# Performance work log

Measured on AMD Instinct MI355X. Metric: run time of the kernel, lower is better.

Reference implementation:

```python
import jax, jax.numpy as jnp
import numpy as np

N_NODES = 100000
N_EDGES = 640000
IN_CH = 128
OUT_CH = 128


def setup_inputs() -> dict:
    key = jax.random.key(0)
    k1, k2, k3, k4, k5, k6 = jax.random.split(key, 6)
    row = jax.random.randint(k1, (N_EDGES,), 0, N_NODES, dtype=jnp.int64 if jax.config.jax_enable_x64 else jnp.int32)
    col = jax.random.randint(k2, (N_EDGES,), 0, N_NODES, dtype=jnp.int64 if jax.config.jax_enable_x64 else jnp.int32)
    vals = jax.random.uniform(k3, (N_EDGES,), dtype=jnp.float32)
    X = jax.random.normal(k4, (N_NODES, IN_CH), dtype=jnp.float32)
    weights = jax.random.normal(k5, (IN_CH, OUT_CH), dtype=jnp.float32)
    bias = jax.random.normal(k6, (OUT_CH,), dtype=jnp.float32)
    return {"row": row, "col": col, "vals": vals, "X": X, "weights": weights, "bias": bias}


def reference(row, col, vals, X, weights, bias):
    # A is sparse COO: A[row[e], col[e]] = vals[e]
    N = X.shape[0]
    # dense feature transform: [N, out]
    XTheta = X @ weights
    # D = (row_sum(A) + 1)^(-1/2)
    deg = jax.ops.segment_sum(vals, row, num_segments=N)
    D = jax.lax.rsqrt(deg + 1.0)
    # Xprime = D * (A @ (D * XTheta))
    Y = D[:, None] * XTheta                                    # [N, out]
    msgs = vals[:, None] * Y[col]                              # [E, out] gather
    AY = jax.ops.segment_sum(msgs, row, num_segments=N)        # [N, out] scatter-add
    return D[:, None] * AY + bias
```

## Files before the change

### kernel.cpp

```cpp
#include <hip/hip_runtime.h>
#include <hip/hip_bf16.h>


#define N_CH 128
#define WT_LD 136
#define FIXS 16777216.0f

typedef __attribute__((ext_vector_type(8))) short short8;
typedef __attribute__((ext_vector_type(4))) float f32x4;
typedef __attribute__((ext_vector_type(4))) unsigned short ushort4v;

__device__ inline unsigned short f2bf(float f) {
    unsigned u = __float_as_uint(f);
    return (unsigned short)((u + 0x7FFFu + ((u >> 16) & 1u)) >> 16);
}
__device__ inline float bf2f(unsigned short h) {
    return __uint_as_float(((unsigned)h) << 16);
}

__global__ __launch_bounds__(256) void rank_kernel(const int* __restrict__ row,
                                                   const float* __restrict__ vals,
                                                   unsigned long long* __restrict__ packed,
                                                   int* __restrict__ rank,
                                                   const float* __restrict__ W,
                                                   unsigned short* __restrict__ Wt,
                                                   int E, int rankBlocks) {
    if ((int)blockIdx.x >= rankBlocks) {
        int i = (blockIdx.x - rankBlocks) * 256 + threadIdx.x;
        int k = i >> 7, n = i & 127;
        Wt[n * N_CH + k] = f2bf(W[k * N_CH + n]);
        return;
    }
    int e0 = blockIdx.x * 512 + threadIdx.x;
#pragma unroll
    for (int j = 0; j < 2; ++j) {
        int e = e0 + j * 256;
        if (e < E) {
            int r = row[e];
            unsigned fx = (unsigned)(vals[e] * FIXS);
            unsigned long long old =
                atomicAdd(&packed[r], (1ULL << 32) | (unsigned long long)fx);
            rank[e] = (int)(old >> 32);
        }
    }
}

__global__ __launch_bounds__(256) void scan1_kernel(const unsigned long long* __restrict__ packed,
                                                    int* __restrict__ pos,
                                                    int* __restrict__ bsum, int N) {
    __shared__ int s[256];
    int t = threadIdx.x;
    int i = blockIdx.x * 256 + t;
    int v = (i < N) ? (int)(packed[i] >> 32) : 0;
    s[t] = v;
    __syncthreads();
    for (int off = 1; off < 256; off <<= 1) {
        int x = (t >= off) ? s[t - off] : 0;
        __syncthreads();
        s[t] += x;
        __syncthreads();
    }
    if (i < N) pos[i] = s[t] - v;
    if (t == 255) bsum[blockIdx.x] = s[t];
}

__global__ __launch_bounds__(256) void scan3_kernel(int* __restrict__ pos,
                                                    const int* __restrict__ bsum,
                                                    const unsigned long long* __restrict__ packed,
                                                    float* __restrict__ dinv, int N) {
    __shared__ int s[256];
    int t = threadIdx.x;
    int b = blockIdx.x;
    int acc = 0;
    for (int j = t; j < b; j += 256) acc += bsum[j];
    s[t] = acc;
    __syncthreads();
    for (int off = 128; off > 0; off >>= 1) {
        if (t < off) s[t] += s[t + off];
        __syncthreads();
    }
    int i = b * 256 + t;
    if (i < N) {
        pos[i] += s[0];
        float deg = (float)(unsigned)(packed[i] & 0xFFFFFFFFull) * (1.0f / FIXS);
        dinv[i] = rsqrtf(deg + 1.0f);
    }
}

__global__ __launch_bounds__(256) void gemm_place_kernel(
        const float* __restrict__ X, const unsigned short* __restrict__ Wt,
        const float* __restrict__ dinv, unsigned short* __restrict__ Ybf, int N,
        const int* __restrict__ row, const int* __restrict__ col,
        const float* __restrict__ vals, const int* __restrict__ pos,
        const int* __restrict__ rank, uint2* __restrict__ epack, int E,
        int gemmBlocks) {
    __shared__ unsigned short Wl[N_CH * WT_LD];

    if ((int)blockIdx.x >= gemmBlocks) {
        int e0 = (blockIdx.x - gemmBlocks) * 1024 + threadIdx.x;
#pragma unroll
        for (int j = 0; j < 4; ++j) {
            int e = e0 + j * 256;
            if (e < E) {
                int r = row[e];
                int p = pos[r] + rank[e];
                epack[p] = make_uint2((unsigned)col[e], __float_as_uint(vals[e]));
            }
        }
        return;
    }

    const int t = threadIdx.x;
    const short8* Wg = (const short8*)Wt;
#pragma unroll
    for (int j = 0; j < 8; ++j) {
        int idx = t + 256 * j;
        int r = idx >> 4, cc = idx & 15;
        *(short8*)(Wl + r * WT_LD + cc * 8) = Wg[idx];
    }
    __syncthreads();

    const int lane = t & 63;
    const int wv = t >> 6;
    const int m = lane & 15;
    const int q = lane >> 4;

#pragma unroll
    for (int i = 0; i < 2; ++i) {
        const int base = (blockIdx.x * 8 + wv * 2 + i) * 16;
        if (base >= N) break;

        short8 a[4];
        const float* xrow = X + (size_t)(base + m) * N_CH + q * 8;
#pragma unroll
        for (int c = 0; c < 4; ++c) {
            f32x4 lo = *(const f32x4*)(xrow + c * 32);
            f32x4 hi = *(const f32x4*)(xrow + c * 32 + 4);
            short8 v;
            v[0] = (short)f2bf(lo[0]); v[1] = (short)f2bf(lo[1]);
            v[2] = (short)f2bf(lo[2]); v[3] = (short)f2bf(lo[3]);
            v[4] = (short)f2bf(hi[0]); v[5] = (short)f2bf(hi[1]);
            v[6] = (short)f2bf(hi[2]); v[7] = (short)f2bf(hi[3]);
            a[c] = v;
        }

        f32x4 acc[8];
#pragma unroll
        for (int tt = 0; tt < 8; ++tt) acc[tt] = (f32x4){0.f, 0.f, 0.f, 0.f};

#pragma unroll
        for (int tt = 0; tt < 8; ++tt) {
            const unsigned short* wrow = Wl + (tt * 16 + m) * WT_LD + q * 8;
#pragma unroll
            for (int c = 0; c < 4; ++c) {
                short8 b = *(const short8*)(wrow + c * 32);
                acc[tt] = __builtin_amdgcn_mfma_f32_16x16x32_bf16(b, a[c], acc[tt], 0, 0, 0);
            }
        }

        const float d = dinv[base + m];
        unsigned short* yrow = Ybf + (size_t)(base + m) * N_CH;
#pragma unroll
        for (int tt = 0; tt < 8; ++tt) {
            unsigned lo = (unsigned)f2bf(acc[tt][0] * d) |
                          ((unsigned)f2bf(acc[tt][1] * d) << 16);
            unsigned hi = (unsigned)f2bf(acc[tt][2] * d) |
                          ((unsigned)f2bf(acc[tt][3] * d) << 16);
            *(uint2*)(yrow + tt * 16 + q * 4) = make_uint2(lo, hi);
        }
    }
}

__global__ __launch_bounds__(256) void gather_kernel(const int* __restrict__ pos,
                                                     const uint2* __restrict__ epack,
                                                     const unsigned short* __restrict__ Ybf,
                                                     const float* __restrict__ dinv,
                                                     const float* __restrict__ bias,
                                                     float* __restrict__ out, int N, int E) {
    unsigned gid = blockIdx.x * 256u + threadIdx.x;
    int n = gid >> 5;
    if (n >= N) return;
    int lane = gid & 31;
    int c = lane * 4;

    int e = pos[n];
    int end = (n + 1 < N) ? pos[n + 1] : E;

    float4 acc = make_float4(0.f, 0.f, 0.f, 0.f);
    for (; e + 4 <= end; e += 4) {
        uint2 p0 = epack[e + 0];
        uint2 p1 = epack[e + 1];
        uint2 p2 = epack[e + 2];
        uint2 p3 = epack[e + 3];
        ushort4v y0 = *(const ushort4v*)(Ybf + (size_t)p0.x * N_CH + c);
        ushort4v y1 = *(const ushort4v*)(Ybf + (size_t)p1.x * N_CH + c);
        ushort4v y2 = *(const ushort4v*)(Ybf + (size_t)p2.x * N_CH + c);
        ushort4v y3 = *(const ushort4v*)(Ybf + (size_t)p3.x * N_CH + c);
        float v0 = __uint_as_float(p0.y);
        float v1 = __uint_as_float(p1.y);
        float v2 = __uint_as_float(p2.y);
        float v3 = __uint_as_float(p3.y);
        acc.x += v0 * bf2f(y0[0]) + v1 * bf2f(y1[0]) + v2 * bf2f(y2[0]) + v3 * bf2f(y3[0]);
        acc.y += v0 * bf2f(y0[1]) + v1 * bf2f(y1[1]) + v2 * bf2f(y2[1]) + v3 * bf2f(y3[1]);
        acc.z += v0 * bf2f(y0[2]) + v1 * bf2f(y1[2]) + v2 * bf2f(y2[2]) + v3 * bf2f(y3[2]);
        acc.w += v0 * bf2f(y0[3]) + v1 * bf2f(y1[3]) + v2 * bf2f(y2[3]) + v3 * bf2f(y3[3]);
    }
    for (; e < end; ++e) {
        uint2 p = epack[e];
        float v = __uint_as_float(p.y);
        ushort4v y = *(const ushort4v*)(Ybf + (size_t)p.x * N_CH + c);
        acc.x += v * bf2f(y[0]);
        acc.y += v * bf2f(y[1]);
        acc.z += v * bf2f(y[2]);
        acc.w += v * bf2f(y[3]);
    }

    float d = dinv[n];
    float4 b = ((const float4*)bias)[lane];
    float4 o;
    o.x = acc.x * d + b.x;
    o.y = acc.y * d + b.y;
    o.z = acc.z * d + b.z;
    o.w = acc.w * d + b.w;
    ((float4*)(out + (size_t)n * N_CH))[lane] = o;
}

extern "C" void kernel_launch(void* const* d_in, const int* in_sizes, int n_in,
                              void* d_out, int out_size, void* d_ws, size_t ws_size,
                              hipStream_t stream) {
    const int*   row  = (const int*)d_in[0];
    const int*   col  = (const int*)d_in[1];
    const float* vals = (const float*)d_in[2];
    const float* X    = (const float*)d_in[3];
    const float* W    = (const float*)d_in[4];
    const float* bias = (const float*)d_in[5];
    float* out = (float*)d_out;

    const int E = in_sizes[0];
    const int N = in_sizes[3] / N_CH;
    const int nb = (N + 255) / 256;

    uint2*              epack  = (uint2*)d_ws;
    unsigned short*     Ybf    = (unsigned short*)(epack + E);
    float*              dinv   = (float*)(Ybf + (size_t)N * N_CH);
    unsigned long long* packed = (unsigned long long*)(dinv + N);
    int*                pos    = (int*)(packed + N);
    int*                rank   = pos + N;
    int*                bsum   = rank + E;
    unsigned short*     Wt     = (unsigned short*)(bsum + nb);

    hipMemsetAsync(packed, 0, (size_t)N * sizeof(unsigned long long), stream);

    const int rankBlocks = (E + 511) / 512;
    rank_kernel<<<rankBlocks + 64, 256, 0, stream>>>(row, vals, packed, rank, W, Wt,
                                                     E, rankBlocks);
    scan1_kernel<<<nb, 256, 0, stream>>>(packed, pos, bsum, N);
    scan3_kernel<<<nb, 256, 0, stream>>>(pos, bsum, packed, dinv, N);

    int tiles = (N + 15) / 16;
    int gemmBlocks = (tiles + 7) / 8;
    int placeBlocks = (E + 1023) / 1024;
    gemm_place_kernel<<<gemmBlocks + placeBlocks, 256, 0, stream>>>(
        X, Wt, dinv, Ybf, N, row, col, vals, pos, rank, epack, E, gemmBlocks);

    unsigned gth = (unsigned)N * 32u;
    gather_kernel<<<(gth + 255) / 256, 256, 0, stream>>>(pos, epack, Ybf, dinv, bias, out, N, E);
}
```

Before: 205.0 us.

## Make GEMM persistent with grid-stride tiles and register-prefetch next X tile

The GEMM portion of the fused gemm/place kernel now launches a fixed 512 blocks. Each wave loops over 16-row tiles with a grid stride, loading the next tile's X rows into registers while the current tile's MFMAs and stores run. It also clamps out-of-range rows and guards the stores for a partial last tile. This is meant to hide global load latency and cut the cost of staging W into LDS once per block. In exchange it uses more registers and has far fewer GEMM waves available to hide latency.

```diff
diff --git a/kernel.cpp b/kernel.cpp
--- a/kernel.cpp
+++ b/kernel.cpp
@@ -125,22 +125,47 @@
     const int m = lane & 15;
     const int q = lane >> 4;
 
-#pragma unroll
-    for (int i = 0; i < 2; ++i) {
-        const int base = (blockIdx.x * 8 + wv * 2 + i) * 16;
-        if (base >= N) break;
+    const int tiles = (N + 15) / 16;
+    const int totalWaves = gemmBlocks * 4;
+    int tile = blockIdx.x * 4 + wv;
+    if (tile >= tiles) return;
+
+    f32x4 pl[4], ph[4];
+    {
+        int rr = tile * 16 + m;
+        if (rr >= N) rr = N - 1;
+        const float* xr = X + (size_t)rr * N_CH + q * 8;
+#pragma unroll
+        for (int c = 0; c < 4; ++c) {
+            pl[c] = *(const f32x4*)(xr + c * 32);
+            ph[c] = *(const f32x4*)(xr + c * 32 + 4);
+        }
+    }
+
+    while (true) {
+        const int next = tile + totalWaves;
+        const bool hasNext = next < tiles;
+
+        f32x4 ql[4], qh[4];
+        if (hasNext) {
+            int rr2 = next * 16 + m;
+            if (rr2 >= N) rr2 = N - 1;
+            const float* xr2 = X + (size_t)rr2 * N_CH + q * 8;
+#pragma unroll
+            for (int c = 0; c < 4; ++c) {
+                ql[c] = *(const f32x4*)(xr2 + c * 32);
+                qh[c] = *(const f32x4*)(xr2 + c * 32 + 4);
+            }
+        }
 
         short8 a[4];
-        const float* xrow = X + (size_t)(base + m) * N_CH + q * 8;
 #pragma unroll
         for (int c = 0; c < 4; ++c) {
-            f32x4 lo = *(const f32x4*)(xrow + c * 32);
-            f32x4 hi = *(const f32x4*)(xrow + c * 32 + 4);
             short8 v;
-            v[0] = (short)f2bf(lo[0]); v[1] = (short)f2bf(lo[1]);
-            v[2] = (short)f2bf(lo[2]); v[3] = (short)f2bf(lo[3]);
-            v[4] = (short)f2bf(hi[0]); v[5] = (short)f2bf(hi[1]);
-            v[6] = (short)f2bf(hi[2]); v[7] = (short)f2bf(hi[3]);
+            v[0] = (short)f2bf(pl[c][0]); v[1] = (short)f2bf(pl[c][1]);
+            v[2] = (short)f2bf(pl[c][2]); v[3] = (short)f2bf(pl[c][3]);
+            v[4] = (short)f2bf(ph[c][0]); v[5] = (short)f2bf(ph[c][1]);
+            v[6] = (short)f2bf(ph[c][2]); v[7] = (short)f2bf(ph[c][3]);
             a[c] = v;
         }
 
@@ -158,16 +183,24 @@
             }
         }
 
-        const float d = dinv[base + m];
-        unsigned short* yrow = Ybf + (size_t)(base + m) * N_CH;
-#pragma unroll
-        for (int tt = 0; tt < 8; ++tt) {
-            unsigned lo = (unsigned)f2bf(acc[tt][0] * d) |
-                          ((unsigned)f2bf(acc[tt][1] * d) << 16);
-            unsigned hi = (unsigned)f2bf(acc[tt][2] * d) |
-                          ((unsigned)f2bf(acc[tt][3] * d) << 16);
-            *(uint2*)(yrow + tt * 16 + q * 4) = make_uint2(lo, hi);
-        }
+        const int rr = tile * 16 + m;
+        if (rr < N) {
+            const float d = dinv[rr];
+            unsigned short* yrow = Ybf + (size_t)rr * N_CH;
+#pragma unroll
+            for (int tt = 0; tt < 8; ++tt) {
+                unsigned lo = (unsigned)f2bf(acc[tt][0] * d) |
+                              ((unsigned)f2bf(acc[tt][1] * d) << 16);
+                unsigned hi = (unsigned)f2bf(acc[tt][2] * d) |
+                              ((unsigned)f2bf(acc[tt][3] * d) << 16);
+                *(uint2*)(yrow + tt * 16 + q * 4) = make_uint2(lo, hi);
+            }
+        }
+
+        if (!hasNext) break;
+#pragma unroll
+        for (int c = 0; c < 4; ++c) { pl[c] = ql[c]; ph[c] = qh[c]; }
+        tile = next;
     }
 }
 
@@ -257,8 +290,7 @@
     scan1_kernel<<<nb, 256, 0, stream>>>(packed, pos, bsum, N);
     scan3_kernel<<<nb, 256, 0, stream>>>(pos, bsum, packed, dinv, N);
 
-    int tiles = (N + 15) / 16;
-    int gemmBlocks = (tiles + 7) / 8;
+    const int gemmBlocks = 512;
     int placeBlocks = (E + 1023) / 1024;
     gemm_place_kernel<<<gemmBlocks + placeBlocks, 256, 0, stream>>>(
         X, Wt, dinv, Ybf, N, row, col, vals, pos, rank, epack, E, gemmBlocks);
```

New measurement: 202.8 us. Within noise of the previous version (-1.1%).
